# Optimization experiments

Hardware: AMD Instinct MI355X
Metric: run time of the kernel (lower is better)

## Reference

```python
import jax, jax.numpy as jnp
import numpy as np

N = 100000   # nodes
E = 1600000  # edges
FEAT = 128
HID = 128
TGT = 64
L = 3
G = 512      # graphs in batch


def setup_inputs() -> dict:
    key = jax.random.key(0)
    ks = jax.random.split(key, 16)
    s = 0.05
    return {
        "x": jax.random.normal(ks[0], (N, FEAT), jnp.float32),
        "edge_index": jax.random.randint(ks[1], (2, E), 0, N, dtype=jnp.int32),
        "batch": jnp.sort(jax.random.randint(ks[2], (N,), 0, G, dtype=jnp.int32)),
        "conv_w1": jax.random.normal(ks[3], (L, FEAT, HID), jnp.float32) * s,
        "conv_b1": jax.random.normal(ks[4], (L, HID), jnp.float32) * s,
        "conv_w2": jax.random.normal(ks[5], (L, HID, HID), jnp.float32) * s,
        "conv_b2": jax.random.normal(ks[6], (L, HID), jnp.float32) * s,
        "eps": jnp.zeros((L,), jnp.float32),
        "gn_scale": jnp.ones((L, HID), jnp.float32),
        "gn_weight": jnp.ones((L, HID), jnp.float32),
        "gn_bias": jnp.zeros((L, HID), jnp.float32),
        "proj_w1": jax.random.normal(ks[7], (L, HID, HID), jnp.float32) * s,
        "proj_b1": jax.random.normal(ks[8], (L, HID), jnp.float32) * s,
        "proj_w2": jax.random.normal(ks[9], (L, HID, TGT), jnp.float32) * s,
        "proj_b2": jax.random.normal(ks[10], (L, TGT), jnp.float32) * s,
    }


def _graph_norm(h, batch, counts, scale, weight, bias):
    # per-graph mean -> scatter back to nodes
    mean = jax.ops.segment_sum(h, batch, num_segments=G) / counts
    sub = h - mean[batch] * scale
    var = jax.ops.segment_sum(sub * sub, batch, num_segments=G) / counts
    std = jnp.sqrt(var + 1e-8)
    return weight * sub / std[batch] + bias


def reference(x, edge_index, batch, conv_w1, conv_b1, conv_w2, conv_b2, eps,
              gn_scale, gn_weight, gn_bias, proj_w1, proj_b1, proj_w2, proj_b2):
    src, dst = edge_index[0], edge_index[1]
    counts = jnp.maximum(
        jax.ops.segment_sum(jnp.ones((N, 1), x.dtype), batch, num_segments=G), 1.0)
    h = x
    z_cat = []
    for l in range(L):
        # GINConv: aggr_j->i then 2-layer MLP
        aggr = jax.ops.segment_sum(h[src], dst, num_segments=N)
        h = (1.0 + eps[l]) * h + aggr
        h = jax.nn.relu(h @ conv_w1[l] + conv_b1[l]) @ conv_w2[l] + conv_b2[l]
        # GraphNorm
        h = _graph_norm(h, batch, counts, gn_scale[l], gn_weight[l], gn_bias[l])
        h = jax.nn.relu(h)
        # projection MLP + global add pool
        z = jax.nn.relu(h @ proj_w1[l] + proj_b1[l]) @ proj_w2[l] + proj_b2[l]
        z_cat.append(jax.ops.segment_sum(z, batch, num_segments=G))
    return jnp.concatenate(z_cat, axis=-1)  # [G, L*TGT]
```

## Files before the change

kernel.cpp:

```cpp
#include <hip/hip_runtime.h>

#define NN 100000
#define EE 1600000
#define HIDD 128
#define TGTT 64
#define GGG 512
#define NBK 98
#define CAPB 17408
#define ABLK 200
#define LSTR 136
#define CVTB 3125
#define GBLK 782
#define OUTB 128

typedef unsigned short ushort_t;
typedef __attribute__((ext_vector_type(8))) short short8;
typedef __attribute__((ext_vector_type(4))) float f32x4;
typedef __attribute__((ext_vector_type(4))) unsigned short us4;

__device__ __forceinline__ float b2f(ushort_t u) {
    union { unsigned int i; float f; } v; v.i = ((unsigned int)u) << 16; return v.f;
}
__device__ __forceinline__ ushort_t f2b(float f) {
    union { float f; unsigned int i; } v; v.f = f;
    unsigned int r = (v.i + 0x7fffu + ((v.i >> 16) & 1u)) >> 16;
    return (ushort_t)r;
}

__global__ __launch_bounds__(256) void k_pro(const float* __restrict__ x, ushort_t* __restrict__ Xb,
                                             const float* __restrict__ cw1, const float* __restrict__ cw2,
                                             const float* __restrict__ pw1, ushort_t* __restrict__ Wt,
                                             const int* __restrict__ batch, int* __restrict__ goff,
                                             const int* __restrict__ ei, int* __restrict__ gcnt,
                                             unsigned int* __restrict__ bbuf) {
    __shared__ ushort_t sW[128 * 129];
    __shared__ int cnt[NBK], base[NBK], cur[NBK];
    int b = blockIdx.x, t = threadIdx.x;

    if (b < CVTB) {
        long i0 = (long)b * 1024 + t;
#pragma unroll
        for (int c = 0; c < 4; c++) {
            long i = i0 + c * 256;
            float4 v = ((const float4*)x)[i];
            us4 o; o.x = f2b(v.x); o.y = f2b(v.y); o.z = f2b(v.z); o.w = f2b(v.w);
            ((us4*)Xb)[i] = o;
        }
        return;
    }
    b -= CVTB;
    if (b < 9) {
        int l = b / 3, j = b % 3;
        const float* src = (j == 0 ? cw1 : j == 1 ? cw2 : pw1) + (size_t)l * HIDD * HIDD;
        ushort_t* dst = Wt + (size_t)b * HIDD * HIDD;
        for (int i = t; i < HIDD * HIDD; i += 256) {
            int k = i >> 7, n = i & 127;
            sW[n * 129 + k] = f2b(src[i]);
        }
        __syncthreads();
        for (int i = t; i < HIDD * HIDD; i += 256) {
            dst[i] = sW[(i >> 7) * 129 + (i & 127)];
        }
        return;
    }
    b -= 9;
    if (b < 3) {
        int g = b * 256 + t;
        if (g > GGG) return;
        int lo = 0, hi = NN;
        while (lo < hi) { int mid = (lo + hi) >> 1; if (batch[mid] < g) lo = mid + 1; else hi = mid; }
        goff[g] = lo;
        return;
    }
    b -= 3;
    {
        if (t < NBK) cnt[t] = 0;
        __syncthreads();
        int e0 = b * 8000;
        int e1 = min(e0 + 8000, EE);
        for (int e = e0 + t; e < e1; e += 256)
            atomicAdd(&cnt[ei[EE + e] >> 10], 1);
        __syncthreads();
        if (t < NBK) { base[t] = atomicAdd(&gcnt[t], cnt[t]); cur[t] = 0; }
        __syncthreads();
        for (int e = e0 + t; e < e1; e += 256) {
            int s = ei[e], d = ei[EE + e];
            int bk = d >> 10;
            int off = base[bk] + atomicAdd(&cur[bk], 1);
            if (off < CAPB)
                bbuf[(long)bk * CAPB + off] = (unsigned int)s | (((unsigned int)d & 1023u) << 17);
        }
    }
}

__global__ __launch_bounds__(256) void k_csr(const int* __restrict__ gcnt,
                                             const unsigned int* __restrict__ bbuf,
                                             int* __restrict__ rowptr, int* __restrict__ csr) {
    __shared__ int ldeg[1024], lcur[1024], tsum[256], sb[NBK];
    int b = blockIdx.x, t = threadIdx.x;
    if (t < NBK) sb[t] = gcnt[t];
    __syncthreads();
    if (t == 0) { int a = 0; for (int i = 0; i < NBK; i++) { int v = sb[i]; sb[i] = a; a += v; } }
    __syncthreads();
    int cnt = min(gcnt[b], CAPB);
    int base = sb[b];
    const unsigned int* bb = bbuf + (long)b * CAPB;
#pragma unroll
    for (int i = 0; i < 4; i++) ldeg[t + 256 * i] = 0;
    __syncthreads();
    for (int i = t; i < cnt; i += 256) atomicAdd(&ldeg[bb[i] >> 17], 1);
    __syncthreads();
    int d0 = ldeg[4 * t], d1 = ldeg[4 * t + 1], d2 = ldeg[4 * t + 2], d3 = ldeg[4 * t + 3];
    int tot = d0 + d1 + d2 + d3;
    tsum[t] = tot;
    __syncthreads();
    for (int off = 1; off < 256; off <<= 1) {
        int u = (t >= off) ? tsum[t - off] : 0;
        __syncthreads();
        tsum[t] += u;
        __syncthreads();
    }
    int texcl = tsum[t] - tot;
    int p0 = base + texcl, p1 = p0 + d0, p2 = p1 + d1, p3 = p2 + d2;
    lcur[4 * t] = p0; lcur[4 * t + 1] = p1; lcur[4 * t + 2] = p2; lcur[4 * t + 3] = p3;
    int gnode = b * 1024 + 4 * t;
    if (gnode < NN)     rowptr[gnode]     = p0;
    if (gnode + 1 < NN) rowptr[gnode + 1] = p1;
    if (gnode + 2 < NN) rowptr[gnode + 2] = p2;
    if (gnode + 3 < NN) rowptr[gnode + 3] = p3;
    if (b == NBK - 1 && t == 0) rowptr[NN] = EE;
    __syncthreads();
    for (int i = t; i < cnt; i += 256) {
        unsigned int en = bb[i];
        int pos = atomicAdd(&lcur[en >> 17], 1);
        csr[pos] = (int)(en & 0x1FFFFu);
    }
}

__global__ __launch_bounds__(256) void k_gmlp(const ushort_t* __restrict__ hin,
                                              const int* __restrict__ rowptr,
                                              const int* __restrict__ csr,
                                              const float* __restrict__ eps, int l,
                                              const ushort_t* __restrict__ Wt1, const float* __restrict__ B1,
                                              const ushort_t* __restrict__ Wt2, const float* __restrict__ B2,
                                              ushort_t* __restrict__ Y,
                                              const float* __restrict__ pooledP, const int* __restrict__ goff,
                                              const float* __restrict__ WoP, const float* __restrict__ BoP,
                                              float* __restrict__ outP, int lprev) {
    __shared__ ushort_t sX[128 * LSTR];
    int tid = threadIdx.x;

    if (blockIdx.x >= GBLK) {
        if (lprev < 0) return;
        int ob = blockIdx.x - GBLK;
        int sub = tid >> 6, tt = tid & 63;
        int g = ob * 4 + sub;
        if (g >= GGG) return;
        float cntg = (float)(goff[g + 1] - goff[g]);
        float acc = cntg * BoP[tt];
        const float* p = pooledP + (long)g * HIDD;
        for (int k = 0; k < HIDD; k++) acc += p[k] * WoP[k * TGTT + tt];
        outP[(long)g * (3 * TGTT) + lprev * TGTT + tt] = acc;
        return;
    }

    long base = (long)blockIdx.x * 128;
    int lane = tid & 15, ng = tid >> 4;
    int off = lane << 3;
    float e1 = 1.0f + eps[l];

#pragma unroll 1
    for (int it = 0; it < 8; it++) {
        int row = it * 16 + ng;
        long node = base + row;
        short8 o = (short8)0;
        if (node < NN) {
            short8 h = *(const short8*)(hin + (node << 7) + off);
            float acc[8];
#pragma unroll
            for (int t = 0; t < 8; t++) acc[t] = e1 * b2f((ushort_t)h[t]);
            int jb = rowptr[node], je = rowptr[node + 1];
            int j = jb;
            for (; j + 8 <= je; j += 8) {
                int s0 = csr[j], s1 = csr[j + 1], s2 = csr[j + 2], s3 = csr[j + 3];
                int s4 = csr[j + 4], s5 = csr[j + 5], s6 = csr[j + 6], s7 = csr[j + 7];
                short8 v0 = *(const short8*)(hin + ((long)s0 << 7) + off);
                short8 v1 = *(const short8*)(hin + ((long)s1 << 7) + off);
                short8 v2 = *(const short8*)(hin + ((long)s2 << 7) + off);
                short8 v3 = *(const short8*)(hin + ((long)s3 << 7) + off);
                short8 v4 = *(const short8*)(hin + ((long)s4 << 7) + off);
                short8 v5 = *(const short8*)(hin + ((long)s5 << 7) + off);
                short8 v6 = *(const short8*)(hin + ((long)s6 << 7) + off);
                short8 v7 = *(const short8*)(hin + ((long)s7 << 7) + off);
#pragma unroll
                for (int t = 0; t < 8; t++)
                    acc[t] += ((b2f((ushort_t)v0[t]) + b2f((ushort_t)v1[t])) +
                               (b2f((ushort_t)v2[t]) + b2f((ushort_t)v3[t]))) +
                              ((b2f((ushort_t)v4[t]) + b2f((ushort_t)v5[t])) +
                               (b2f((ushort_t)v6[t]) + b2f((ushort_t)v7[t])));
            }
            for (; j + 4 <= je; j += 4) {
                int s0 = csr[j], s1 = csr[j + 1], s2 = csr[j + 2], s3 = csr[j + 3];
                short8 v0 = *(const short8*)(hin + ((long)s0 << 7) + off);
                short8 v1 = *(const short8*)(hin + ((long)s1 << 7) + off);
                short8 v2 = *(const short8*)(hin + ((long)s2 << 7) + off);
                short8 v3 = *(const short8*)(hin + ((long)s3 << 7) + off);
#pragma unroll
                for (int t = 0; t < 8; t++)
                    acc[t] += (b2f((ushort_t)v0[t]) + b2f((ushort_t)v1[t])) +
                              (b2f((ushort_t)v2[t]) + b2f((ushort_t)v3[t]));
            }
            for (; j < je; j++) {
                int s = csr[j];
                short8 v = *(const short8*)(hin + ((long)s << 7) + off);
#pragma unroll
                for (int t = 0; t < 8; t++) acc[t] += b2f((ushort_t)v[t]);
            }
#pragma unroll
            for (int t = 0; t < 8; t++) o[t] = (short)f2b(acc[t]);
        }
        *(short8*)(sX + row * LSTR + off) = o;
    }
    __syncthreads();

    int w = tid >> 6, l64 = tid & 63, q = l64 >> 4, l16 = l64 & 15;
    int r0 = w * 16, r1 = 64 + w * 16;
    short8 a0[4], a1[4];
#pragma unroll
    for (int c = 0; c < 4; c++) {
        a0[c] = *(const short8*)(sX + (r0 + l16) * LSTR + q * 8 + c * 32);
        a1[c] = *(const short8*)(sX + (r1 + l16) * LSTR + q * 8 + c * 32);
    }
    f32x4 acc0[8], acc1[8];
#pragma unroll
    for (int nt = 0; nt < 8; nt++) {
        int col = nt * 16 + l16;
        float bias = B1[col];
        f32x4 c0 = {bias, bias, bias, bias};
        f32x4 c1 = c0;
        const ushort_t* bB = Wt1 + col * HIDD + q * 8;
#pragma unroll
        for (int c = 0; c < 4; c++) {
            short8 b = *(const short8*)(bB + c * 32);
            c0 = __builtin_amdgcn_mfma_f32_16x16x32_bf16(a0[c], b, c0, 0, 0, 0);
            c1 = __builtin_amdgcn_mfma_f32_16x16x32_bf16(a1[c], b, c1, 0, 0, 0);
        }
        acc0[nt] = c0; acc1[nt] = c1;
    }
#pragma unroll
    for (int nt = 0; nt < 8; nt++) {
        int col = nt * 16 + l16;
#pragma unroll
        for (int r = 0; r < 4; r++) {
            sX[(r0 + q * 4 + r) * LSTR + col] = f2b(fmaxf(acc0[nt][r], 0.f));
            sX[(r1 + q * 4 + r) * LSTR + col] = f2b(fmaxf(acc1[nt][r], 0.f));
        }
    }
#pragma unroll
    for (int c = 0; c < 4; c++) {
        a0[c] = *(const short8*)(sX + (r0 + l16) * LSTR + q * 8 + c * 32);
        a1[c] = *(const short8*)(sX + (r1 + l16) * LSTR + q * 8 + c * 32);
    }
#pragma unroll
    for (int nt = 0; nt < 8; nt++) {
        int col = nt * 16 + l16;
        float bias = B2[col];
        f32x4 c0 = {bias, bias, bias, bias};
        f32x4 c1 = c0;
        const ushort_t* bB = Wt2 + col * HIDD + q * 8;
#pragma unroll
        for (int c = 0; c < 4; c++) {
            short8 b = *(const short8*)(bB + c * 32);
            c0 = __builtin_amdgcn_mfma_f32_16x16x32_bf16(a0[c], b, c0, 0, 0, 0);
            c1 = __builtin_amdgcn_mfma_f32_16x16x32_bf16(a1[c], b, c1, 0, 0, 0);
        }
#pragma unroll
        for (int r = 0; r < 4; r++) {
            long row0 = base + r0 + q * 4 + r;
            long row1 = base + r1 + q * 4 + r;
            if (row0 < NN) Y[(row0 << 7) + col] = f2b(c0[r]);
            if (row1 < NN) Y[(row1 << 7) + col] = f2b(c1[r]);
        }
    }
}

__global__ __launch_bounds__(512) void k_gstat(const ushort_t* __restrict__ Hraw,
                                               const int* __restrict__ goff,
                                               const float* __restrict__ scale,
                                               const float* __restrict__ weight,
                                               float* __restrict__ msb, float* __restrict__ invb,
                                               float* __restrict__ pooled) {
    __shared__ float red[2][32][128];
    int g = blockIdx.x;
    int s = goff[g], e = goff[g + 1];
    float cnt = (float)max(e - s, 1);
    int lane = threadIdx.x & 15;
    int rg = threadIdx.x >> 4;
    int f0 = lane << 3;
    float sum[8], sq[8];
#pragma unroll
    for (int t = 0; t < 8; t++) { sum[t] = 0.f; sq[t] = 0.f; }
    for (int i = s + rg; i < e; i += 32) {
        short8 v = *(const short8*)(Hraw + ((long)i << 7) + f0);
#pragma unroll
        for (int t = 0; t < 8; t++) { float a = b2f((ushort_t)v[t]); sum[t] += a; sq[t] += a * a; }
    }
#pragma unroll
    for (int t = 0; t < 8; t++) { red[0][rg][f0 + t] = sum[t]; red[1][rg][f0 + t] = sq[t]; }
    __syncthreads();
    for (int off = 16; off > 0; off >>= 1) {
        if (rg < off) {
#pragma unroll
            for (int t = 0; t < 8; t++) {
                red[0][rg][f0 + t] += red[0][rg + off][f0 + t];
                red[1][rg][f0 + t] += red[1][rg + off][f0 + t];
            }
        }
        __syncthreads();
    }
    if (rg == 0) {
#pragma unroll
        for (int t = 0; t < 8; t++) {
            int f = f0 + t;
            float mean = red[0][0][f] / cnt;
            float ms = mean * scale[f];
            float var = red[1][0][f] / cnt - 2.f * ms * mean + ms * ms;
            msb[g * HIDD + f] = ms;
            invb[g * HIDD + f] = weight[f] / sqrtf(var + 1e-8f);
            pooled[g * HIDD + f] = 0.f;
        }
    }
}

__global__ __launch_bounds__(256) void k_projpool(const ushort_t* __restrict__ Hraw,
                                                  const int* __restrict__ batch,
                                                  const float* __restrict__ msb, const float* __restrict__ invb,
                                                  const float* __restrict__ gnb,
                                                  const ushort_t* __restrict__ Wt, const float* __restrict__ B,
                                                  ushort_t* __restrict__ Hn, float* __restrict__ pooled,
                                                  int store_hn) {
    __shared__ ushort_t sX[128 * LSTR];
    __shared__ int sgid[128];
    int tid = threadIdx.x;
    long base = (long)blockIdx.x * 128;
#pragma unroll
    for (int c = 0; c < 8; c++) {
        int idx = c * 256 + tid;
        int row = idx >> 4, cw = idx & 15;
        long grow = base + row;
        short8 v = (short8)0;
        if (grow < NN) {
            short8 raw = *(const short8*)(Hraw + (grow << 7) + (cw << 3));
            int g = batch[grow];
            if (cw == 0) sgid[row] = g;
            const float* msp = msb + g * HIDD + (cw << 3);
            const float* ivp = invb + g * HIDD + (cw << 3);
            const float* gbp = gnb + (cw << 3);
            float4 m0 = *(const float4*)msp, m1 = *(const float4*)(msp + 4);
            float4 i0 = *(const float4*)ivp, i1 = *(const float4*)(ivp + 4);
            float4 g0 = *(const float4*)gbp, g1 = *(const float4*)(gbp + 4);
            float mv[8] = {m0.x, m0.y, m0.z, m0.w, m1.x, m1.y, m1.z, m1.w};
            float iv[8] = {i0.x, i0.y, i0.z, i0.w, i1.x, i1.y, i1.z, i1.w};
            float gv[8] = {g0.x, g0.y, g0.z, g0.w, g1.x, g1.y, g1.z, g1.w};
#pragma unroll
            for (int t = 0; t < 8; t++) {
                float val = (b2f((ushort_t)raw[t]) - mv[t]) * iv[t] + gv[t];
                v[t] = (short)f2b(val > 0.f ? val : 0.f);
            }
            if (store_hn) *(short8*)(Hn + (grow << 7) + (cw << 3)) = v;
        } else if (cw == 0) {
            sgid[row] = -1;
        }
        *(short8*)(sX + row * LSTR + (cw << 3)) = v;
    }
    __syncthreads();

    int w = tid >> 6, l64 = tid & 63, q = l64 >> 4, l16 = l64 & 15;
    int r0 = w * 16, r1 = 64 + w * 16;
    short8 a0[4], a1[4];
#pragma unroll
    for (int c = 0; c < 4; c++) {
        a0[c] = *(const short8*)(sX + (r0 + l16) * LSTR + q * 8 + c * 32);
        a1[c] = *(const short8*)(sX + (r1 + l16) * LSTR + q * 8 + c * 32);
    }
    f32x4 acc0[8], acc1[8];
#pragma unroll
    for (int nt = 0; nt < 8; nt++) {
        int col = nt * 16 + l16;
        float bias = B[col];
        f32x4 c0 = {bias, bias, bias, bias};
        f32x4 c1 = c0;
        const ushort_t* bB = Wt + col * HIDD + q * 8;
#pragma unroll
        for (int c = 0; c < 4; c++) {
            short8 b = *(const short8*)(bB + c * 32);
            c0 = __builtin_amdgcn_mfma_f32_16x16x32_bf16(a0[c], b, c0, 0, 0, 0);
            c1 = __builtin_amdgcn_mfma_f32_16x16x32_bf16(a1[c], b, c1, 0, 0, 0);
        }
        acc0[nt] = c0; acc1[nt] = c1;
    }
#pragma unroll
    for (int nt = 0; nt < 8; nt++) {
        int col = nt * 16 + l16;
#pragma unroll
        for (int r = 0; r < 4; r++) {
            sX[(r0 + q * 4 + r) * LSTR + col] = f2b(fmaxf(acc0[nt][r], 0.f));
            sX[(r1 + q * 4 + r) * LSTR + col] = f2b(fmaxf(acc1[nt][r], 0.f));
        }
    }
    __syncthreads();

    int f = tid & 127, half = tid >> 7;
    int rbeg = half * 64, rend = rbeg + 64;
    float sum = 0.f;
    int curg = -1;
    for (int row = rbeg; row < rend; row++) {
        int g = sgid[row];
        if (g != curg) {
            if (curg >= 0) atomicAdd(&pooled[(long)curg * HIDD + f], sum);
            sum = 0.f; curg = g;
        }
        if (g >= 0) sum += b2f(sX[row * LSTR + f]);
    }
    if (curg >= 0) atomicAdd(&pooled[(long)curg * HIDD + f], sum);
}

__global__ __launch_bounds__(256) void k_out(const float* __restrict__ pooled, const int* __restrict__ goff,
                                             const float* __restrict__ W, const float* __restrict__ B,
                                             float* __restrict__ out, int l) {
    int sub = threadIdx.x >> 6, tt = threadIdx.x & 63;
    int g = blockIdx.x * 4 + sub;
    if (g >= GGG) return;
    float cnt = (float)(goff[g + 1] - goff[g]);
    float acc = cnt * B[tt];
    const float* p = pooled + (long)g * HIDD;
    for (int k = 0; k < HIDD; k++) acc += p[k] * W[k * TGTT + tt];
    out[(long)g * (3 * TGTT) + l * TGTT + tt] = acc;
}

extern "C" void kernel_launch(void* const* d_in, const int* in_sizes, int n_in,
                              void* d_out, int out_size, void* d_ws, size_t ws_size,
                              hipStream_t stream) {
    const float* x    = (const float*)d_in[0];
    const int*   ei   = (const int*)d_in[1];
    const int*   batch= (const int*)d_in[2];
    const float* cw1  = (const float*)d_in[3];
    const float* cb1  = (const float*)d_in[4];
    const float* cw2  = (const float*)d_in[5];
    const float* cb2  = (const float*)d_in[6];
    const float* eps  = (const float*)d_in[7];
    const float* gsc  = (const float*)d_in[8];
    const float* gw   = (const float*)d_in[9];
    const float* gb   = (const float*)d_in[10];
    const float* pw1  = (const float*)d_in[11];
    const float* pb1  = (const float*)d_in[12];
    const float* pw2  = (const float*)d_in[13];
    const float* pb2  = (const float*)d_in[14];
    float* out = (float*)d_out;

    ushort_t* Xb   = (ushort_t*)d_ws;
    ushort_t* Hn   = Xb;
    ushort_t* Hraw = Xb + (size_t)NN * HIDD;
    ushort_t* Wt   = Hraw + (size_t)NN * HIDD;
    float* msb     = (float*)(Wt + (size_t)9 * HIDD * HIDD);
    float* invb    = msb + (size_t)GGG * HIDD;
    float* pooled  = invb + (size_t)GGG * HIDD;
    int* goff   = (int*)(pooled + (size_t)GGG * HIDD);
    int* rowptr = goff + (GGG + 1);
    int* gcnt   = rowptr + (NN + 1);
    int* csr    = gcnt + NBK;
    unsigned int* bbuf = (unsigned int*)(csr + EE);

    hipMemsetAsync(gcnt, 0, NBK * sizeof(int), stream);
    k_pro<<<CVTB + 9 + 3 + ABLK, 256, 0, stream>>>(x, Xb, cw1, cw2, pw1, Wt, batch, goff, ei, gcnt, bbuf);
    k_csr<<<NBK, 256, 0, stream>>>(gcnt, bbuf, rowptr, csr);

    for (int l = 0; l < 3; l++) {
        const ushort_t* hin = (l == 0) ? Xb : Hn;
        ushort_t* Wt1 = Wt + (size_t)(l * 3 + 0) * HIDD * HIDD;
        ushort_t* Wt2 = Wt + (size_t)(l * 3 + 1) * HIDD * HIDD;
        ushort_t* Wtp = Wt + (size_t)(l * 3 + 2) * HIDD * HIDD;
        int grid = GBLK + (l > 0 ? OUTB : 0);
        k_gmlp<<<grid, 256, 0, stream>>>(hin, rowptr, csr, eps, l,
                                         Wt1, cb1 + l * HIDD, Wt2, cb2 + l * HIDD, Hraw,
                                         pooled, goff,
                                         pw2 + (size_t)(l - 1) * HIDD * TGTT, pb2 + (l - 1) * TGTT,
                                         out, l - 1);
        k_gstat<<<GGG, 512, 0, stream>>>(Hraw, goff, gsc + l * HIDD, gw + l * HIDD, msb, invb, pooled);
        k_projpool<<<GBLK, 256, 0, stream>>>(Hraw, batch, msb, invb, gb + l * HIDD,
                                             Wtp, pb1 + l * HIDD, Hn, pooled, (l < 2) ? 1 : 0);
    }
    k_out<<<OUTB, 256, 0, stream>>>(pooled, goff, pw2 + (size_t)2 * HIDD * TGTT, pb2 + 2 * TGTT, out, 2);
}
```

Measured before the change: 608.8 us.

## Split fused gather+MLP kernel into separate gather and MFMA MLP kernels

The fused per-layer kernel that gathered neighbour features into shared memory and then ran the two-layer MLP is split in two. A gather kernel now handles 64 nodes per block with no shared memory and an occupancy hint, writing the aggregated bf16 rows to a global buffer. An MLP kernel then loads 128-row tiles from that buffer and runs the matrix multiplies in place. The aim is higher occupancy for the latency-bound gather, at the cost of an extra global round trip and one more launch per layer.

```diff
diff --git a/kernel.cpp b/kernel.cpp
--- a/kernel.cpp
+++ b/kernel.cpp
@@ -10,7 +10,9 @@
 #define ABLK 200
 #define LSTR 136
 #define CVTB 3125
-#define GBLK 782
+#define GBLKG 1563
+#define GBLKM 782
+#define FOUTB 128
 #define OUTB 128
 
 typedef unsigned short ushort_t;
@@ -137,22 +139,19 @@
     }
 }
 
-__global__ __launch_bounds__(256) void k_gmlp(const ushort_t* __restrict__ hin,
-                                              const int* __restrict__ rowptr,
-                                              const int* __restrict__ csr,
-                                              const float* __restrict__ eps, int l,
-                                              const ushort_t* __restrict__ Wt1, const float* __restrict__ B1,
-                                              const ushort_t* __restrict__ Wt2, const float* __restrict__ B2,
-                                              ushort_t* __restrict__ Y,
-                                              const float* __restrict__ pooledP, const int* __restrict__ goff,
-                                              const float* __restrict__ WoP, const float* __restrict__ BoP,
-                                              float* __restrict__ outP, int lprev) {
-    __shared__ ushort_t sX[128 * LSTR];
+__global__ __launch_bounds__(256, 8) void k_gather(const ushort_t* __restrict__ hin,
+                                                   const int* __restrict__ rowptr,
+                                                   const int* __restrict__ csr,
+                                                   const float* __restrict__ eps, int l,
+                                                   ushort_t* __restrict__ aggr,
+                                                   const float* __restrict__ pooledP, const int* __restrict__ goff,
+                                                   const float* __restrict__ WoP, const float* __restrict__ BoP,
+                                                   float* __restrict__ outP, int lprev) {
     int tid = threadIdx.x;
 
-    if (blockIdx.x >= GBLK) {
+    if (blockIdx.x >= GBLKG) {
         if (lprev < 0) return;
-        int ob = blockIdx.x - GBLK;
+        int ob = blockIdx.x - GBLKG;
         int sub = tid >> 6, tt = tid & 63;
         int g = ob * 4 + sub;
         if (g >= GGG) return;
@@ -164,16 +163,15 @@
         return;
     }
 
-    long base = (long)blockIdx.x * 128;
+    long base = (long)blockIdx.x * 64;
     int lane = tid & 15, ng = tid >> 4;
     int off = lane << 3;
     float e1 = 1.0f + eps[l];
 
 #pragma unroll 1
-    for (int it = 0; it < 8; it++) {
+    for (int it = 0; it < 4; it++) {
         int row = it * 16 + ng;
         long node = base + row;
-        short8 o = (short8)0;
         if (node < NN) {
             short8 h = *(const short8*)(hin + (node << 7) + off);
             float acc[8];
@@ -216,10 +214,30 @@
 #pragma unroll
                 for (int t = 0; t < 8; t++) acc[t] += b2f((ushort_t)v[t]);
             }
+            short8 o;
 #pragma unroll
             for (int t = 0; t < 8; t++) o[t] = (short)f2b(acc[t]);
-        }
-        *(short8*)(sX + row * LSTR + off) = o;
+            *(short8*)(aggr + (node << 7) + off) = o;
+        }
+    }
+}
+
+__global__ __launch_bounds__(256) void k_mlp(const ushort_t* __restrict__ aggr,
+                                             const ushort_t* __restrict__ Wt1, const float* __restrict__ B1,
+                                             const ushort_t* __restrict__ Wt2, const float* __restrict__ B2,
+                                             ushort_t* __restrict__ Y) {
+    __shared__ ushort_t sX[128 * LSTR];
+    int tid = threadIdx.x;
+    long base = (long)blockIdx.x * 128;
+
+#pragma unroll
+    for (int c = 0; c < 8; c++) {
+        int idx = c * 256 + tid;
+        int row = idx >> 4, cw = idx & 15;
+        long grow = base + row;
+        short8 v = (short8)0;
+        if (grow < NN) v = *(const short8*)(aggr + (grow << 7) + (cw << 3));
+        *(short8*)(sX + row * LSTR + (cw << 3)) = v;
     }
     __syncthreads();
 
@@ -480,15 +498,15 @@
         ushort_t* Wt1 = Wt + (size_t)(l * 3 + 0) * HIDD * HIDD;
         ushort_t* Wt2 = Wt + (size_t)(l * 3 + 1) * HIDD * HIDD;
         ushort_t* Wtp = Wt + (size_t)(l * 3 + 2) * HIDD * HIDD;
-        int grid = GBLK + (l > 0 ? OUTB : 0);
-        k_gmlp<<<grid, 256, 0, stream>>>(hin, rowptr, csr, eps, l,
-                                         Wt1, cb1 + l * HIDD, Wt2, cb2 + l * HIDD, Hraw,
-                                         pooled, goff,
-                                         pw2 + (size_t)(l - 1) * HIDD * TGTT, pb2 + (l - 1) * TGTT,
-                                         out, l - 1);
+        int grid = GBLKG + (l > 0 ? FOUTB : 0);
+        k_gather<<<grid, 256, 0, stream>>>(hin, rowptr, csr, eps, l, Hraw,
+                                           pooled, goff,
+                                           pw2 + (size_t)(l - 1) * HIDD * TGTT, pb2 + (l - 1) * TGTT,
+                                           out, l - 1);
+        k_mlp<<<GBLKM, 256, 0, stream>>>(Hraw, Wt1, cb1 + l * HIDD, Wt2, cb2 + l * HIDD, Hraw);
         k_gstat<<<GGG, 512, 0, stream>>>(Hraw, goff, gsc + l * HIDD, gw + l * HIDD, msb, invb, pooled);
-        k_projpool<<<GBLK, 256, 0, stream>>>(Hraw, batch, msb, invb, gb + l * HIDD,
-                                             Wtp, pb1 + l * HIDD, Hn, pooled, (l < 2) ? 1 : 0);
+        k_projpool<<<GBLKM, 256, 0, stream>>>(Hraw, batch, msb, invb, gb + l * HIDD,
+                                              Wtp, pb1 + l * HIDD, Hn, pooled, (l < 2) ? 1 : 0);
     }
     k_out<<<OUTB, 256, 0, stream>>>(pooled, goff, pw2 + (size_t)2 * HIDD * TGTT, pb2 + 2 * TGTT, out, 2);
 }
```

New measurement: 632.8 us. 1.04x slower.
